# Kernel tuning notes

Hardware: AMD Instinct MI355X
Metric: run time of the kernel (lower is better)

Reference implementation:

```python
import jax, jax.numpy as jnp
import numpy as np

HEADS1, HID = 2, 128
OUT_FEATS = 256
K, M = 8, 128


def _gat_conv(x, src, dst, W, a_src, a_dst, bias, heads, out_dim, concat, neg_slope):
    """PyG-style GATConv: linear -> per-edge leakyrelu attention -> dst-softmax -> scatter-sum."""
    N = x.shape[0]
    h = (x @ W.T).reshape(N, heads, out_dim)          # [N, H, D]
    alpha_src = jnp.sum(h * a_src, axis=-1)            # [N, H]
    alpha_dst = jnp.sum(h * a_dst, axis=-1)            # [N, H]
    e = jax.nn.leaky_relu(alpha_src[src] + alpha_dst[dst], neg_slope)  # [E, H]
    # numerically stable segment softmax over incoming edges per destination
    m = jax.ops.segment_max(e, dst, num_segments=N)    # [N, H]
    e = jnp.exp(e - m[dst])
    s = jax.ops.segment_sum(e, dst, num_segments=N)    # [N, H]
    alpha = e / s[dst]                                  # [E, H]
    msg = h[src] * alpha[:, :, None]                    # [E, H, D]
    out = jax.ops.segment_sum(msg, dst, num_segments=N)  # [N, H, D]
    out = out.reshape(N, heads * out_dim) if concat else out.mean(axis=1)
    return out + bias


def setup_inputs() -> dict:
    key = jax.random.key(0)
    ks = jax.random.split(key, 14)
    N, E, IN = 50000, 800000, 256
    x = jax.random.normal(ks[0], (N, IN), dtype=jnp.float32)
    edge_index = jax.random.randint(ks[1], (2, E), 0, N, dtype=jnp.int64)
    sc = 0.1
    return {
        "x": x,
        "edge_index": edge_index,
        "W1": jax.random.normal(ks[2], (HEADS1 * HID, IN), dtype=jnp.float32) * sc,
        "a_src1": jax.random.normal(ks[3], (HEADS1, HID), dtype=jnp.float32) * sc,
        "a_dst1": jax.random.normal(ks[4], (HEADS1, HID), dtype=jnp.float32) * sc,
        "b1": jax.random.normal(ks[5], (HEADS1 * HID,), dtype=jnp.float32) * sc,
        "W2": jax.random.normal(ks[6], (OUT_FEATS, HEADS1 * HID), dtype=jnp.float32) * sc,
        "a_src2": jax.random.normal(ks[7], (1, OUT_FEATS), dtype=jnp.float32) * sc,
        "a_dst2": jax.random.normal(ks[8], (1, OUT_FEATS), dtype=jnp.float32) * sc,
        "b2": jax.random.normal(ks[9], (OUT_FEATS,), dtype=jnp.float32) * sc,
        "g": jax.random.normal(ks[10], (OUT_FEATS, K * M), dtype=jnp.float32) * sc,
        "mu": jax.random.normal(ks[11], (K, M), dtype=jnp.float32) * sc,
    }


def reference(x, edge_index, W1, a_src1, a_dst1, b1, W2, a_src2, a_dst2, b2, g, mu):
    N = x.shape[0]
    loops = jnp.arange(N, dtype=edge_index.dtype)  # PyG GATConv adds self-loops by default
    src = jnp.concatenate([edge_index[0], loops])
    dst = jnp.concatenate([edge_index[1], loops])
    h = _gat_conv(x, src, dst, W1, a_src1, a_dst1, b1, HEADS1, HID, True, 0.2)
    h = jax.nn.leaky_relu(h, 0.01)  # F.leaky_relu default slope
    h = _gat_conv(h, src, dst, W2, a_src2, a_dst2, b2, 1, OUT_FEATS, False, 0.2)
    out = (h @ g).reshape(N, K, M)                      # [N, K, M]
    # cosine similarity against mu along M (torch eps=1e-8)
    num = jnp.einsum('nkm,km->nk', out, mu)
    denom = jnp.maximum(
        jnp.linalg.norm(out, axis=-1) * jnp.linalg.norm(mu, axis=-1)[None, :], 1e-8
    )
    return num / denom  # [N, K]
```

## Files before the change

### kernel.cpp

```cpp
#include <hip/hip_runtime.h>
#include <math.h>

typedef short s16x8 __attribute__((ext_vector_type(8)));
typedef float f32x4 __attribute__((ext_vector_type(4)));

__device__ __forceinline__ float lrelu(float x, float s) { return x > 0.0f ? x : s * x; }

__device__ __forceinline__ unsigned short f2bf(float f) {
  unsigned int u = __float_as_uint(f);
  u = (u + 0x7FFFu + ((u >> 16) & 1u)) >> 16;
  return (unsigned short)u;
}
__device__ __forceinline__ float bf2f(unsigned short h) {
  return __uint_as_float(((unsigned int)h) << 16);
}

__device__ __forceinline__ void gload_lds16(void* lds, const void* g) {
  __builtin_amdgcn_global_load_lds(
      (const __attribute__((address_space(1))) unsigned int*)g,
      (__attribute__((address_space(3))) unsigned int*)lds, 16, 0, 0);
}

__global__ void deg_kernel(const int* __restrict__ dst, int* __restrict__ deg, int E) {
  int e = blockIdx.x * blockDim.x + threadIdx.x;
  if (e < E) atomicAdd(&deg[dst[e]], 1);
}

__global__ __launch_bounds__(256) void bsum_kernel(const int* __restrict__ deg,
                                                   int* __restrict__ bsum, int N) {
  int t = blockIdx.x * 256 + threadIdx.x;
  int v = (t < N) ? deg[t] : 0;
  #pragma unroll
  for (int off = 1; off < 64; off <<= 1) v += __shfl_xor(v, off, 64);
  __shared__ int ws[4];
  if ((threadIdx.x & 63) == 0) ws[threadIdx.x >> 6] = v;
  __syncthreads();
  if (threadIdx.x == 0) bsum[blockIdx.x] = ws[0] + ws[1] + ws[2] + ws[3];
}

__global__ __launch_bounds__(256) void bscan_kernel(const int* __restrict__ bsum,
                                                    int* __restrict__ boff, int nb,
                                                    int* __restrict__ rowptr_total) {
  __shared__ int s[256];
  int t = threadIdx.x;
  int v = (t < nb) ? bsum[t] : 0;
  s[t] = v;
  __syncthreads();
  for (int off = 1; off < 256; off <<= 1) {
    int u = (t >= off) ? s[t - off] : 0;
    __syncthreads();
    s[t] += u;
    __syncthreads();
  }
  if (t < nb) boff[t] = s[t] - v;
  if (t == nb - 1) *rowptr_total = s[t];
}

__global__ __launch_bounds__(256) void bwrite_kernel(const int* __restrict__ deg,
                                                     const int* __restrict__ boff,
                                                     int* __restrict__ rowptr,
                                                     int* __restrict__ cursor, int N) {
  __shared__ int s[256];
  int t = blockIdx.x * 256 + threadIdx.x;
  int v = (t < N) ? deg[t] : 0;
  s[threadIdx.x] = v;
  __syncthreads();
  for (int off = 1; off < 256; off <<= 1) {
    int u = (threadIdx.x >= off) ? s[threadIdx.x - off] : 0;
    __syncthreads();
    s[threadIdx.x] += u;
    __syncthreads();
  }
  if (t < N) {
    int ex = boff[blockIdx.x] + s[threadIdx.x] - v;
    rowptr[t] = ex;
    cursor[t] = ex;
  }
}

__global__ void fill_kernel(const int* __restrict__ src, const int* __restrict__ dst,
                            int* __restrict__ cursor, int* __restrict__ colsrc, int E) {
  int e = blockIdx.x * blockDim.x + threadIdx.x;
  if (e < E) {
    int d = dst[e];
    int pos = atomicAdd(&cursor[d], 1);
    colsrc[pos] = src[e];
  }
}

__global__ void cvt_rows_kernel(const float* __restrict__ src, unsigned short* __restrict__ dst,
                                int nrows, int prows) {
  int t = blockIdx.x * blockDim.x + threadIdx.x;
  int row = t >> 6;
  int c = (t & 63) * 4;
  if (row >= prows) return;
  float4 v = make_float4(0.f, 0.f, 0.f, 0.f);
  if (row < nrows) v = *(const float4*)&src[(size_t)row * 256 + c];
  ushort4 o;
  o.x = f2bf(v.x); o.y = f2bf(v.y); o.z = f2bf(v.z); o.w = f2bf(v.w);
  *(ushort4*)&dst[(size_t)row * 256 + c] = o;
}

__global__ void cvt_gT_kernel(const float* __restrict__ g, unsigned short* __restrict__ gT) {
  int idx = blockIdx.x * blockDim.x + threadIdx.x;
  int k = idx >> 10, n = idx & 1023;
  gT[(size_t)n * 256 + k] = f2bf(g[idx]);
}

template<int EPI, int AH, int NY>
__global__ __launch_bounds__(256, 2) void gemm_bf16(
    const unsigned short* __restrict__ A, const unsigned short* __restrict__ B,
    unsigned short* __restrict__ Cb,
    const float* __restrict__ avs, const float* __restrict__ avd,
    float* __restrict__ asrcO, float* __restrict__ adstO,
    const float* __restrict__ mu, const float* __restrict__ nmu,
    float* __restrict__ outcos, int M)
{
  __shared__ unsigned short As[128 * 64];
  __shared__ unsigned short Bs[128 * 64];
  const int gm = (M + 127) >> 7;
  const int id = blockIdx.x;
  const int xcd = id & 7;
  const int tt = id >> 3;
  const int j  = tt & (NY - 1);
  const int xg = tt / NY;
  const int xt = xg * 8 + xcd;
  if (xt >= gm) return;
  const int t = threadIdx.x;
  const int w = t >> 6;
  const int l = t & 63;
  const int m0 = xt * 128;
  const int n0 = j * 128;

  f32x4 acc[2][8];
  #pragma unroll
  for (int i = 0; i < 2; ++i)
    #pragma unroll
    for (int jj = 0; jj < 8; ++jj) acc[i][jj] = (f32x4){0.f, 0.f, 0.f, 0.f};

  const unsigned char* Ab = (const unsigned char*)A;
  const unsigned char* Bb = (const unsigned char*)B;
  unsigned char* AsB = (unsigned char*)As;
  unsigned char* BsB = (unsigned char*)Bs;

  const int srow = l >> 3;
  const int gchk = (l & 7) ^ srow;

  for (int kb = 0; kb < 256; kb += 64) {
    #pragma unroll
    for (int i = 0; i < 4; ++i) {
      int seg = w * 4 + i;
      int row = seg * 8 + srow;
      gload_lds16(AsB + seg * 1024,
                  Ab + (size_t)(m0 + row) * 512 + kb * 2 + gchk * 16);
      gload_lds16(BsB + seg * 1024,
                  Bb + (size_t)(n0 + row) * 512 + kb * 2 + gchk * 16);
    }
    asm volatile("s_waitcnt vmcnt(0)" ::: "memory");
    __syncthreads();

    const int rl = l & 15;
    const int kc = l >> 4;
    #pragma unroll
    for (int ks = 0; ks < 2; ++ks) {
      s16x8 af[2], bfr[8];
      #pragma unroll
      for (int mf = 0; mf < 2; ++mf) {
        int r = w * 32 + mf * 16 + rl;
        int slot = (ks * 4 + kc) ^ (r & 7);
        af[mf] = *(const s16x8*)&As[r * 64 + slot * 8];
      }
      #pragma unroll
      for (int nf = 0; nf < 8; ++nf) {
        int r = nf * 16 + rl;
        int slot = (ks * 4 + kc) ^ (r & 7);
        bfr[nf] = *(const s16x8*)&Bs[r * 64 + slot * 8];
      }
      #pragma unroll
      for (int mf = 0; mf < 2; ++mf)
        #pragma unroll
        for (int nf = 0; nf < 8; ++nf)
          acc[mf][nf] = __builtin_amdgcn_mfma_f32_16x16x32_bf16(af[mf], bfr[nf], acc[mf][nf], 0, 0, 0);
    }
    __syncthreads();
  }

  if (EPI == 0) {
    #pragma unroll
    for (int mf = 0; mf < 2; ++mf)
      #pragma unroll
      for (int nf = 0; nf < 8; ++nf)
        #pragma unroll
        for (int jj = 0; jj < 4; ++jj) {
          int r = m0 + w * 32 + mf * 16 + (l >> 4) * 4 + jj;
          int c = n0 + nf * 16 + (l & 15);
          Cb[(size_t)r * 256 + c] = f2bf(acc[mf][nf][jj]);
        }
    if (AH > 0) {
      float avS[8], avD[8];
      #pragma unroll
      for (int nf = 0; nf < 8; ++nf) {
        avS[nf] = avs[n0 + nf * 16 + (l & 15)];
        avD[nf] = avd[n0 + nf * 16 + (l & 15)];
      }
      #pragma unroll
      for (int mf = 0; mf < 2; ++mf)
        #pragma unroll
        for (int jj = 0; jj < 4; ++jj) {
          float ds = 0.f, dd = 0.f;
          #pragma unroll
          for (int nf = 0; nf < 8; ++nf) {
            float o = acc[mf][nf][jj];
            ds = fmaf(o, avS[nf], ds);
            dd = fmaf(o, avD[nf], dd);
          }
          #pragma unroll
          for (int off = 1; off < 16; off <<= 1) {
            ds += __shfl_xor(ds, off, 64);
            dd += __shfl_xor(dd, off, 64);
          }
          if ((l & 15) == 0) {
            int r = m0 + w * 32 + mf * 16 + (l >> 4) * 4 + jj;
            if (r < M) {
              if (AH == 2) {
                asrcO[(size_t)r * 2 + j] = ds;
                adstO[(size_t)r * 2 + j] = dd;
              } else {
                atomicAdd(&asrcO[r], ds);
                atomicAdd(&adstO[r], dd);
              }
            }
          }
        }
    }
  } else {
    const int kchunk = j;
    float nm = nmu[kchunk];
    float mv[8];
    #pragma unroll
    for (int nf = 0; nf < 8; ++nf) mv[nf] = mu[kchunk * 128 + nf * 16 + (l & 15)];
    #pragma unroll
    for (int mf = 0; mf < 2; ++mf)
      #pragma unroll
      for (int jj = 0; jj < 4; ++jj) {
        float num = 0.f, ss = 0.f;
        #pragma unroll
        for (int nf = 0; nf < 8; ++nf) {
          float o = acc[mf][nf][jj];
          num = fmaf(o, mv[nf], num);
          ss  = fmaf(o, o, ss);
        }
        #pragma unroll
        for (int off = 1; off < 16; off <<= 1) {
          num += __shfl_xor(num, off, 64);
          ss  += __shfl_xor(ss, off, 64);
        }
        if ((l & 15) == 0) {
          int r = m0 + w * 32 + mf * 16 + (l >> 4) * 4 + jj;
          if (r < M) outcos[(size_t)r * 8 + kchunk] = num / fmaxf(sqrtf(ss) * nm, 1e-8f);
        }
      }
  }
}

template<int H, bool OUT_LRELU>
__global__ __launch_bounds__(256) void agg_kernel(
    const unsigned short* __restrict__ hin, const float* __restrict__ asrc,
    const float* __restrict__ adst, const int* __restrict__ rowptr,
    const int* __restrict__ colsrc, const float* __restrict__ bias,
    unsigned short* __restrict__ outp, int N)
{
  int wid  = threadIdx.x >> 6;
  int lane = threadIdx.x & 63;
  int n = blockIdx.x * 4 + wid;
  if (n >= N) return;
  const int half = lane >> 5;
  const int fl   = lane & 31;
  const int head = (H == 2) ? (fl >> 4) : 0;

  int beg = rowptr[n], end = rowptr[n + 1];

  float ad0 = adst[(size_t)n * H + 0];
  float ad1 = (H == 2) ? adst[(size_t)n * 2 + 1] : 0.f;
  float m0 = lrelu(asrc[(size_t)n * H + 0] + ad0, 0.2f);
  float m1 = (H == 2) ? lrelu(asrc[(size_t)n * 2 + 1] + ad1, 0.2f) : 0.f;
  float s0 = 1.f, s1 = 1.f;

  float acc[8];
  {
    s16x8 hv = *(const s16x8*)&hin[(size_t)n * 256 + fl * 8];
    #pragma unroll
    for (int k = 0; k < 8; ++k)
      acc[k] = (half == 0) ? bf2f((unsigned short)hv[k]) : 0.f;
  }

  for (int cbeg = beg; cbeg < end; cbeg += 64) {
    int cnt = end - cbeg; if (cnt > 64) cnt = 64;
    int src_i = 0;
    float e0 = -1e30f, e1 = -1e30f;
    if (lane < cnt) {
      src_i = colsrc[cbeg + lane];
      if (H == 2) {
        float2 av = *(const float2*)&asrc[(size_t)src_i * 2];
        e0 = lrelu(av.x + ad0, 0.2f);
        e1 = lrelu(av.y + ad1, 0.2f);
      } else {
        e0 = lrelu(asrc[src_i] + ad0, 0.2f);
      }
    }
    float c0 = e0, c1 = e1;
    #pragma unroll
    for (int off = 32; off >= 1; off >>= 1) {
      c0 = fmaxf(c0, __shfl_xor(c0, off, 64));
      if (H == 2) c1 = fmaxf(c1, __shfl_xor(c1, off, 64));
    }
    float nm0 = fmaxf(m0, c0);
    float r0 = __expf(m0 - nm0); m0 = nm0;
    float r1 = 1.f;
    if (H == 2) { float nm1 = fmaxf(m1, c1); r1 = __expf(m1 - nm1); m1 = nm1; }
    s0 *= r0; if (H == 2) s1 *= r1;
    float rh = (H == 2 && head) ? r1 : r0;
    #pragma unroll
    for (int k = 0; k < 8; ++k) acc[k] *= rh;
    float p0 = (lane < cnt) ? __expf(e0 - m0) : 0.f;
    float p1 = (H == 2 && lane < cnt) ? __expf(e1 - m1) : 0.f;
    float t0 = p0, t1 = p1;
    #pragma unroll
    for (int off = 32; off >= 1; off >>= 1) {
      t0 += __shfl_xor(t0, off, 64);
      if (H == 2) t1 += __shfl_xor(t1, off, 64);
    }
    s0 += t0; if (H == 2) s1 += t1;

    int npair = (cnt + 1) >> 1;
    int npr = (npair + 3) & ~3;
    for (int pi = 0; pi < npr; pi += 4) {
      int sj[4]; float wv[4];
      #pragma unroll
      for (int u = 0; u < 4; ++u) {
        int e = (pi + u) * 2 + half;
        sj[u] = __shfl(src_i, e, 64);
        float q0 = __shfl(p0, e, 64);
        if (H == 2) {
          float q1 = __shfl(p1, e, 64);
          wv[u] = head ? q1 : q0;
        } else {
          wv[u] = q0;
        }
      }
      s16x8 v0 = *(const s16x8*)&hin[(size_t)sj[0] * 256 + fl * 8];
      s16x8 v1 = *(const s16x8*)&hin[(size_t)sj[1] * 256 + fl * 8];
      s16x8 v2 = *(const s16x8*)&hin[(size_t)sj[2] * 256 + fl * 8];
      s16x8 v3 = *(const s16x8*)&hin[(size_t)sj[3] * 256 + fl * 8];
      #pragma unroll
      for (int k = 0; k < 8; ++k) acc[k] = fmaf(bf2f((unsigned short)v0[k]), wv[0], acc[k]);
      #pragma unroll
      for (int k = 0; k < 8; ++k) acc[k] = fmaf(bf2f((unsigned short)v1[k]), wv[1], acc[k]);
      #pragma unroll
      for (int k = 0; k < 8; ++k) acc[k] = fmaf(bf2f((unsigned short)v2[k]), wv[2], acc[k]);
      #pragma unroll
      for (int k = 0; k < 8; ++k) acc[k] = fmaf(bf2f((unsigned short)v3[k]), wv[3], acc[k]);
    }
  }

  float sh = (H == 2 && head) ? s1 : s0;
  float inv = 1.0f / sh;
  #pragma unroll
  for (int k = 0; k < 8; ++k) acc[k] += __shfl_xor(acc[k], 32, 64);
  if (half == 0) {
    float bv[8];
    *(float4*)&bv[0] = *(const float4*)&bias[fl * 8];
    *(float4*)&bv[4] = *(const float4*)&bias[fl * 8 + 4];
    s16x8 o;
    #pragma unroll
    for (int k = 0; k < 8; ++k) {
      float v = acc[k] * inv + bv[k];
      if (OUT_LRELU) v = lrelu(v, 0.01f);
      o[k] = (short)f2bf(v);
    }
    *(s16x8*)&outp[(size_t)n * 256 + fl * 8] = o;
  }
}

__global__ __launch_bounds__(64) void munorm_kernel(const float* __restrict__ mu,
                                                    float* __restrict__ norm_mu) {
  int lane = threadIdx.x;
  for (int k = 0; k < 8; ++k) {
    float v0 = mu[k * 128 + lane];
    float v1 = mu[k * 128 + 64 + lane];
    float s = v0 * v0 + v1 * v1;
    #pragma unroll
    for (int off = 1; off < 64; off <<= 1) s += __shfl_xor(s, off, 64);
    if (lane == 0) norm_mu[k] = sqrtf(s);
  }
}

extern "C" void kernel_launch(void* const* d_in, const int* in_sizes, int n_in,
                              void* d_out, int out_size, void* d_ws, size_t ws_size,
                              hipStream_t stream) {
  const float* x      = (const float*)d_in[0];
  const int*   ei     = (const int*)  d_in[1];
  const float* W1     = (const float*)d_in[2];
  const float* a_src1 = (const float*)d_in[3];
  const float* a_dst1 = (const float*)d_in[4];
  const float* b1     = (const float*)d_in[5];
  const float* W2     = (const float*)d_in[6];
  const float* a_src2 = (const float*)d_in[7];
  const float* a_dst2 = (const float*)d_in[8];
  const float* b2     = (const float*)d_in[9];
  const float* g      = (const float*)d_in[10];
  const float* mu     = (const float*)d_in[11];

  const int N  = in_sizes[0] / 256;
  const int E  = in_sizes[1] / 2;
  const int Mp = ((N + 127) / 128) * 128;
  const int nb = (N + 255) / 256;
  const int* src = ei;
  const int* dst = ei + E;

  unsigned short* us = (unsigned short*)d_ws;
  size_t off = 0;
  unsigned short* xb  = us + off; off += (size_t)Mp * 256;
  unsigned short* h1b = us + off; off += (size_t)Mp * 256;
  unsigned short* o1b = us + off; off += (size_t)Mp * 256;
  unsigned short* h2b = us + off; off += (size_t)Mp * 256;
  unsigned short* o2b = xb;
  float* f = (float*)(us + off);
  size_t fo = 0;
  float* asrc1 = f + fo; fo += (size_t)N * 2;
  float* adst1 = f + fo; fo += (size_t)N * 2;
  float* asrc2 = f + fo; fo += N;
  float* adst2 = f + fo; fo += N;
  float* nmu   = f + fo; fo += 8;
  int* deg    = (int*)(f + fo);
  int* rowptr = deg + N;
  int* cursor = rowptr + N + 1;
  int* colsrc = cursor + N;
  int* bsum   = colsrc + E;
  int* boff   = bsum + 256;
  unsigned short* w1b = (unsigned short*)(boff + 256);
  unsigned short* w2b = w1b + 256 * 256;
  unsigned short* gTb = w2b + 256 * 256;

  hipMemsetAsync(deg, 0, (size_t)N * sizeof(int), stream);
  hipMemsetAsync(asrc2, 0, (size_t)N * 2 * sizeof(float), stream);
  deg_kernel<<<(E + 255) / 256, 256, 0, stream>>>(dst, deg, E);
  bsum_kernel<<<nb, 256, 0, stream>>>(deg, bsum, N);
  bscan_kernel<<<1, 256, 0, stream>>>(bsum, boff, nb, rowptr + N);
  bwrite_kernel<<<nb, 256, 0, stream>>>(deg, boff, rowptr, cursor, N);
  fill_kernel<<<(E + 255) / 256, 256, 0, stream>>>(src, dst, cursor, colsrc, E);

  cvt_rows_kernel<<<Mp / 4, 256, 0, stream>>>(x, xb, N, Mp);
  cvt_rows_kernel<<<64, 256, 0, stream>>>(W1, w1b, 256, 256);
  cvt_rows_kernel<<<64, 256, 0, stream>>>(W2, w2b, 256, 256);
  cvt_gT_kernel<<<1024, 256, 0, stream>>>(g, gTb);
  munorm_kernel<<<1, 64, 0, stream>>>(mu, nmu);

  const int gm  = Mp / 128;
  const int nxg = (gm + 7) / 8;
  const int g2  = nxg * 8 * 2;
  const int g8  = nxg * 8 * 8;

  gemm_bf16<0, 2, 2><<<g2, 256, 0, stream>>>(xb, w1b, h1b,
      a_src1, a_dst1, asrc1, adst1, nullptr, nullptr, nullptr, N);
  agg_kernel<2, true><<<(N + 3) / 4, 256, 0, stream>>>(h1b, asrc1, adst1, rowptr, colsrc, b1, o1b, N);

  gemm_bf16<0, 1, 2><<<g2, 256, 0, stream>>>(o1b, w2b, h2b,
      a_src2, a_dst2, asrc2, adst2, nullptr, nullptr, nullptr, N);
  agg_kernel<1, false><<<(N + 3) / 4, 256, 0, stream>>>(h2b, asrc2, adst2, rowptr, colsrc, b2, o2b, N);

  gemm_bf16<1, 0, 8><<<g8, 256, 0, stream>>>(o2b, gTb, nullptr,
      nullptr, nullptr, nullptr, nullptr, mu, nmu, (float*)d_out, N);
}
```

Before: 419.0 us.

## Split GAT aggregation into edge-alpha kernel and feature-parallel gather kernel

Replaces the fused online-softmax aggregation kernel with two kernels. The first computes normalized per-edge attention weights and the self-loop weight and stores them to workspace. The second gathers neighbor features, with each wave handling a 64-feature slice of one node and using scalar readlane broadcasts of source index and weight. This drops the online rescaling from the gather loop and spreads each node across four blocks. The cost is extra global traffic for the alpha arrays, a second pass over the edges, and narrower 2-byte loads per lane in the gather.

```diff
diff --git a/kernel.cpp b/kernel.cpp
--- a/kernel.cpp
+++ b/kernel.cpp
@@ -263,49 +263,34 @@
   }
 }
 
-template<int H, bool OUT_LRELU>
-__global__ __launch_bounds__(256) void agg_kernel(
-    const unsigned short* __restrict__ hin, const float* __restrict__ asrc,
-    const float* __restrict__ adst, const int* __restrict__ rowptr,
-    const int* __restrict__ colsrc, const float* __restrict__ bias,
-    unsigned short* __restrict__ outp, int N)
+template<int H>
+__global__ __launch_bounds__(256) void alpha_edge_kernel(
+    const float* __restrict__ asrc, const float* __restrict__ adst,
+    const int* __restrict__ rowptr, const int* __restrict__ colsrc,
+    float* __restrict__ al0, float* __restrict__ al1,
+    float* __restrict__ asl0, float* __restrict__ asl1, int N)
 {
-  int wid  = threadIdx.x >> 6;
-  int lane = threadIdx.x & 63;
+  int wid = threadIdx.x >> 6, lane = threadIdx.x & 63;
   int n = blockIdx.x * 4 + wid;
   if (n >= N) return;
-  const int half = lane >> 5;
-  const int fl   = lane & 31;
-  const int head = (H == 2) ? (fl >> 4) : 0;
-
   int beg = rowptr[n], end = rowptr[n + 1];
-
   float ad0 = adst[(size_t)n * H + 0];
   float ad1 = (H == 2) ? adst[(size_t)n * 2 + 1] : 0.f;
-  float m0 = lrelu(asrc[(size_t)n * H + 0] + ad0, 0.2f);
-  float m1 = (H == 2) ? lrelu(asrc[(size_t)n * 2 + 1] + ad1, 0.2f) : 0.f;
-  float s0 = 1.f, s1 = 1.f;
-
-  float acc[8];
-  {
-    s16x8 hv = *(const s16x8*)&hin[(size_t)n * 256 + fl * 8];
-    #pragma unroll
-    for (int k = 0; k < 8; ++k)
-      acc[k] = (half == 0) ? bf2f((unsigned short)hv[k]) : 0.f;
-  }
+  float self0 = lrelu(asrc[(size_t)n * H + 0] + ad0, 0.2f);
+  float self1 = (H == 2) ? lrelu(asrc[(size_t)n * 2 + 1] + ad1, 0.2f) : 0.f;
+  float m0 = self0, m1 = self1, s0 = 1.f, s1 = 1.f;
 
   for (int cbeg = beg; cbeg < end; cbeg += 64) {
     int cnt = end - cbeg; if (cnt > 64) cnt = 64;
-    int src_i = 0;
     float e0 = -1e30f, e1 = -1e30f;
     if (lane < cnt) {
-      src_i = colsrc[cbeg + lane];
+      int s = colsrc[cbeg + lane];
       if (H == 2) {
-        float2 av = *(const float2*)&asrc[(size_t)src_i * 2];
+        float2 av = *(const float2*)&asrc[(size_t)s * 2];
         e0 = lrelu(av.x + ad0, 0.2f);
         e1 = lrelu(av.y + ad1, 0.2f);
       } else {
-        e0 = lrelu(asrc[src_i] + ad0, 0.2f);
+        e0 = lrelu(asrc[s] + ad0, 0.2f);
       }
     }
     float c0 = e0, c1 = e1;
@@ -314,72 +299,89 @@
       c0 = fmaxf(c0, __shfl_xor(c0, off, 64));
       if (H == 2) c1 = fmaxf(c1, __shfl_xor(c1, off, 64));
     }
-    float nm0 = fmaxf(m0, c0);
-    float r0 = __expf(m0 - nm0); m0 = nm0;
-    float r1 = 1.f;
-    if (H == 2) { float nm1 = fmaxf(m1, c1); r1 = __expf(m1 - nm1); m1 = nm1; }
-    s0 *= r0; if (H == 2) s1 *= r1;
-    float rh = (H == 2 && head) ? r1 : r0;
-    #pragma unroll
-    for (int k = 0; k < 8; ++k) acc[k] *= rh;
+    float nm0 = fmaxf(m0, c0); s0 *= __expf(m0 - nm0); m0 = nm0;
+    if (H == 2) { float nm1 = fmaxf(m1, c1); s1 *= __expf(m1 - nm1); m1 = nm1; }
     float p0 = (lane < cnt) ? __expf(e0 - m0) : 0.f;
     float p1 = (H == 2 && lane < cnt) ? __expf(e1 - m1) : 0.f;
-    float t0 = p0, t1 = p1;
     #pragma unroll
     for (int off = 32; off >= 1; off >>= 1) {
-      t0 += __shfl_xor(t0, off, 64);
-      if (H == 2) t1 += __shfl_xor(t1, off, 64);
-    }
-    s0 += t0; if (H == 2) s1 += t1;
-
-    int npair = (cnt + 1) >> 1;
-    int npr = (npair + 3) & ~3;
-    for (int pi = 0; pi < npr; pi += 4) {
-      int sj[4]; float wv[4];
-      #pragma unroll
-      for (int u = 0; u < 4; ++u) {
-        int e = (pi + u) * 2 + half;
-        sj[u] = __shfl(src_i, e, 64);
-        float q0 = __shfl(p0, e, 64);
-        if (H == 2) {
-          float q1 = __shfl(p1, e, 64);
-          wv[u] = head ? q1 : q0;
-        } else {
-          wv[u] = q0;
-        }
-      }
-      s16x8 v0 = *(const s16x8*)&hin[(size_t)sj[0] * 256 + fl * 8];
-      s16x8 v1 = *(const s16x8*)&hin[(size_t)sj[1] * 256 + fl * 8];
-      s16x8 v2 = *(const s16x8*)&hin[(size_t)sj[2] * 256 + fl * 8];
-      s16x8 v3 = *(const s16x8*)&hin[(size_t)sj[3] * 256 + fl * 8];
-      #pragma unroll
-      for (int k = 0; k < 8; ++k) acc[k] = fmaf(bf2f((unsigned short)v0[k]), wv[0], acc[k]);
-      #pragma unroll
-      for (int k = 0; k < 8; ++k) acc[k] = fmaf(bf2f((unsigned short)v1[k]), wv[1], acc[k]);
-      #pragma unroll
-      for (int k = 0; k < 8; ++k) acc[k] = fmaf(bf2f((unsigned short)v2[k]), wv[2], acc[k]);
-      #pragma unroll
-      for (int k = 0; k < 8; ++k) acc[k] = fmaf(bf2f((unsigned short)v3[k]), wv[3], acc[k]);
-    }
-  }
-
-  float sh = (H == 2 && head) ? s1 : s0;
-  float inv = 1.0f / sh;
-  #pragma unroll
-  for (int k = 0; k < 8; ++k) acc[k] += __shfl_xor(acc[k], 32, 64);
-  if (half == 0) {
-    float bv[8];
-    *(float4*)&bv[0] = *(const float4*)&bias[fl * 8];
-    *(float4*)&bv[4] = *(const float4*)&bias[fl * 8 + 4];
-    s16x8 o;
-    #pragma unroll
-    for (int k = 0; k < 8; ++k) {
-      float v = acc[k] * inv + bv[k];
-      if (OUT_LRELU) v = lrelu(v, 0.01f);
-      o[k] = (short)f2bf(v);
-    }
-    *(s16x8*)&outp[(size_t)n * 256 + fl * 8] = o;
-  }
+      p0 += __shfl_xor(p0, off, 64);
+      if (H == 2) p1 += __shfl_xor(p1, off, 64);
+    }
+    s0 += p0; if (H == 2) s1 += p1;
+  }
+
+  float i0 = 1.f / s0;
+  float i1 = (H == 2) ? 1.f / s1 : 0.f;
+  if (lane == 0) {
+    asl0[n] = __expf(self0 - m0) * i0;
+    if (H == 2) asl1[n] = __expf(self1 - m1) * i1;
+  }
+  for (int cbeg = beg; cbeg < end; cbeg += 64) {
+    int cnt = end - cbeg; if (cnt > 64) cnt = 64;
+    if (lane < cnt) {
+      int s = colsrc[cbeg + lane];
+      if (H == 2) {
+        float2 av = *(const float2*)&asrc[(size_t)s * 2];
+        al0[cbeg + lane] = __expf(lrelu(av.x + ad0, 0.2f) - m0) * i0;
+        al1[cbeg + lane] = __expf(lrelu(av.y + ad1, 0.2f) - m1) * i1;
+      } else {
+        al0[cbeg + lane] = __expf(lrelu(asrc[s] + ad0, 0.2f) - m0) * i0;
+      }
+    }
+  }
+}
+
+template<int H, bool OUT_LRELU>
+__global__ __launch_bounds__(256) void gat_gather_kernel(
+    const unsigned short* __restrict__ hin,
+    const float* __restrict__ al0, const float* __restrict__ al1,
+    const float* __restrict__ asl0, const float* __restrict__ asl1,
+    const int* __restrict__ rowptr, const int* __restrict__ colsrc,
+    const float* __restrict__ bias, unsigned short* __restrict__ outp, int N)
+{
+  const int id = blockIdx.x;
+  const int fg = (id & 7) >> 1;
+  const int sub = id & 1;
+  const int wid = threadIdx.x >> 6, lane = threadIdx.x & 63;
+  const int n = (id >> 3) * 8 + sub * 4 + wid;
+  if (n >= N) return;
+  const int f = fg * 64 + lane;
+  const float* alph = (H == 2 && fg >= 2) ? al1 : al0;
+  const float* aslf = (H == 2 && fg >= 2) ? asl1 : asl0;
+  int beg = rowptr[n], end = rowptr[n + 1];
+
+  float acc = aslf[n] * bf2f(hin[(size_t)n * 256 + f]);
+
+  for (int cbeg = beg; cbeg < end; cbeg += 64) {
+    int cnt = end - cbeg; if (cnt > 64) cnt = 64;
+    int sidx = 0; float aval = 0.f;
+    if (lane < cnt) {
+      sidx = colsrc[cbeg + lane];
+      aval = alph[cbeg + lane];
+    }
+    int nr = (cnt + 7) & ~7;
+    for (int u0 = 0; u0 < nr; u0 += 8) {
+      int ss[8]; float aa[8];
+      #pragma unroll
+      for (int u = 0; u < 8; ++u) {
+        ss[u] = __builtin_amdgcn_readlane(sidx, u0 + u);
+        aa[u] = __uint_as_float(
+            __builtin_amdgcn_readlane((int)__float_as_uint(aval), u0 + u));
+      }
+      float hv[8];
+      #pragma unroll
+      for (int u = 0; u < 8; ++u)
+        hv[u] = bf2f(hin[(size_t)ss[u] * 256 + f]);
+      #pragma unroll
+      for (int u = 0; u < 8; ++u)
+        acc = fmaf(hv[u], aa[u], acc);
+    }
+  }
+
+  float v = acc + bias[f];
+  if (OUT_LRELU) v = lrelu(v, 0.01f);
+  outp[(size_t)n * 256 + f] = f2bf(v);
 }
 
 __global__ __launch_bounds__(64) void munorm_kernel(const float* __restrict__ mu,
@@ -432,6 +434,12 @@
   float* asrc2 = f + fo; fo += N;
   float* adst2 = f + fo; fo += N;
   float* nmu   = f + fo; fo += 8;
+  float* al10  = f + fo; fo += E;
+  float* al11  = f + fo; fo += E;
+  float* al2   = f + fo; fo += E;
+  float* as10  = f + fo; fo += N;
+  float* as11  = f + fo; fo += N;
+  float* as2   = f + fo; fo += N;
   int* deg    = (int*)(f + fo);
   int* rowptr = deg + N;
   int* cursor = rowptr + N + 1;
@@ -460,14 +468,22 @@
   const int nxg = (gm + 7) / 8;
   const int g2  = nxg * 8 * 2;
   const int g8  = nxg * 8 * 8;
+  const int nbk = (N + 7) / 8;
+  const int gg  = nbk * 8;
 
   gemm_bf16<0, 2, 2><<<g2, 256, 0, stream>>>(xb, w1b, h1b,
       a_src1, a_dst1, asrc1, adst1, nullptr, nullptr, nullptr, N);
-  agg_kernel<2, true><<<(N + 3) / 4, 256, 0, stream>>>(h1b, asrc1, adst1, rowptr, colsrc, b1, o1b, N);
+  alpha_edge_kernel<2><<<(N + 3) / 4, 256, 0, stream>>>(
+      asrc1, adst1, rowptr, colsrc, al10, al11, as10, as11, N);
+  gat_gather_kernel<2, true><<<gg, 256, 0, stream>>>(
+      h1b, al10, al11, as10, as11, rowptr, colsrc, b1, o1b, N);
 
   gemm_bf16<0, 1, 2><<<g2, 256, 0, stream>>>(o1b, w2b, h2b,
       a_src2, a_dst2, asrc2, adst2, nullptr, nullptr, nullptr, N);
-  agg_kernel<1, false><<<(N + 3) / 4, 256, 0, stream>>>(h2b, asrc2, adst2, rowptr, colsrc, b2, o2b, N);
+  alpha_edge_kernel<1><<<(N + 3) / 4, 256, 0, stream>>>(
+      asrc2, adst2, rowptr, colsrc, al2, al2, as2, as2, N);
+  gat_gather_kernel<1, false><<<gg, 256, 0, stream>>>(
+      h2b, al2, al2, as2, as2, rowptr, colsrc, b2, o2b, N);
 
   gemm_bf16<1, 0, 8><<<g8, 256, 0, stream>>>(o2b, gTb, nullptr,
       nullptr, nullptr, nullptr, nullptr, mu, nmu, (float*)d_out, N);
```

New measurement: 484.8 us. 1.16x slower.
